# Kernel optimization log

Hardware: AMD Instinct MI355X
Metric: run time of the kernel (lower is better)

## Reference

```python
import jax, jax.numpy as jnp
import numpy as np

B, C_FEAT, H_F, W_F = 16, 256, 80, 80
C_ILL, K, H_Z, W_Z = 64, 3, 40, 40


def setup_inputs() -> dict:
    key = jax.random.key(0)
    k1, k2, k3, k4, k5, k6, k7 = jax.random.split(key, 7)
    feat = jax.random.normal(k1, (B, C_FEAT, H_F, W_F), dtype=jnp.float32)
    Z = jax.random.normal(k2, (B, C_ILL, H_Z, W_Z), dtype=jnp.float32)
    P = jax.random.uniform(k3, (B, K, H_Z, W_Z), dtype=jnp.float32)
    # Expert 1x1-conv params (original zero-inits; use small random for nontrivial math)
    Wg = jax.random.normal(k4, (K, C_FEAT, C_ILL), dtype=jnp.float32) * 0.02
    bg = jax.random.normal(k5, (K, C_FEAT), dtype=jnp.float32) * 0.02
    Wb = jax.random.normal(k6, (K, C_FEAT, C_ILL), dtype=jnp.float32) * 0.02
    bb = jax.random.normal(k7, (K, C_FEAT), dtype=jnp.float32) * 0.02
    return {"feat": feat, "Z": Z, "P": P, "Wg": Wg, "bg": bg, "Wb": Wb, "bb": bb}


def reference(feat, Z, P, Wg, bg, Wb, bb):
    Bb, C, H, W = feat.shape
    # bilinear upsample, half-pixel centers (== torch align_corners=False)
    Z_up = jax.image.resize(Z, (Z.shape[0], Z.shape[1], H, W), method='bilinear')
    P_up = jax.image.resize(P, (P.shape[0], P.shape[1], H, W), method='bilinear')
    # router-weighted illumination features: [B,K,D,H,W]
    ZP = jnp.einsum('bkhw,bdhw->bkdhw', P_up, Z_up)
    # soft-routed 1x1-conv experts, fused across K (weights + router-weighted biases)
    delta_gamma = jnp.einsum('bkdhw,kcd->bchw', ZP, Wg) + jnp.einsum('bkhw,kc->bchw', P_up, bg)
    delta_beta = jnp.einsum('bkdhw,kcd->bchw', ZP, Wb) + jnp.einsum('bkhw,kc->bchw', P_up, bb)
    # FiLM residual modulation
    return feat * (1.0 + delta_gamma) + delta_beta
```

## Files before the change

### kernel.cpp

```cpp
#include <hip/hip_runtime.h>
#include <hip/hip_bf16.h>

#define NB   16
#define NC   256
#define HF   80
#define WF   80
#define NPIX 6400
#define ND   64
#define NK   3
#define HZ   40
#define WZ   40
#define KD   224
#define NKC  7
#define NPB  400
#define ZP_B_STRIDE ((size_t)NPB * NKC * 512)
#define PB_STRIDE   (NKC * 512)
#define A_G_STRIDE  (NKC * 4 * 512)

typedef __bf16 bf16;
typedef __bf16 bf16x8 __attribute__((ext_vector_type(8)));
typedef float  floatx4 __attribute__((ext_vector_type(4)));

__global__ __launch_bounds__(256) void pack_A_kernel(
    const float* __restrict__ Wg, const float* __restrict__ bg,
    const float* __restrict__ Wb, const float* __restrict__ bb,
    bf16* __restrict__ A2)
{
    int i = blockIdx.x * 256 + threadIdx.x;
    int lane = i & 63;
    int j2 = i >> 6;
    int mt = j2 & 3;
    int j3 = j2 >> 2;
    int kc = j3 % 7;
    int g  = j3 / 7;
    int l15 = lane & 15, q = lane >> 4;
    int cbase = (g >> 1) * 64 + (g & 1) * 32;
    int c = cbase + (mt & 1) * 16 + l15;
    const float* W    = (mt >= 2) ? Wb : Wg;
    const float* bias = (mt >= 2) ? bb : bg;
    int kd0 = kc * 32 + q * 8;

    bf16x8 v;
    if (kd0 < NK * ND) {
        int k = kd0 >> 6, d = kd0 & 63;
        const float* src = W + ((size_t)k * NC + c) * ND + d;
        #pragma unroll
        for (int j = 0; j < 8; ++j) v[j] = (bf16)src[j];
    } else if (kd0 == NK * ND) {
        #pragma unroll
        for (int j = 0; j < 8; ++j) v[j] = (bf16)0.0f;
        v[0] = (bf16)bias[0 * NC + c];
        v[1] = (bf16)bias[1 * NC + c];
        v[2] = (bf16)bias[2 * NC + c];
    } else {
        #pragma unroll
        for (int j = 0; j < 8; ++j) v[j] = (bf16)0.0f;
    }
    *reinterpret_cast<bf16x8*>(A2 + (size_t)i * 8) = v;
}

__global__ __launch_bounds__(256) void build_zp_kernel(
    const float* __restrict__ Z, const float* __restrict__ P,
    bf16* __restrict__ ZP2)
{
    __shared__ float z_up[WF][ND + 1];
    __shared__ float p_up[WF][NK];

    const int bid = blockIdx.x;
    const int b   = bid / HF;
    const int h   = bid - b * HF;
    const int t   = threadIdx.x;

    float srch = 0.5f * (float)h - 0.25f;
    float flh  = floorf(srch);
    float fh   = srch - flh;
    int h0 = (int)flh, h1 = h0 + 1;
    h0 = max(h0, 0); h1 = min(h1, HZ - 1);

    #pragma unroll 4
    for (int i = 0; i < 20; ++i) {
        int e = t + 256 * i;
        int d = e / WF;
        int w = e - d * WF;
        float srcw = 0.5f * (float)w - 0.25f;
        float flw  = floorf(srcw);
        float fw   = srcw - flw;
        int w0 = (int)flw, w1 = w0 + 1;
        w0 = max(w0, 0); w1 = min(w1, WZ - 1);
        const float* Zr = Z + (size_t)(b * ND + d) * (HZ * WZ);
        float z00 = Zr[h0 * WZ + w0], z01 = Zr[h0 * WZ + w1];
        float z10 = Zr[h1 * WZ + w0], z11 = Zr[h1 * WZ + w1];
        float zi0 = z00 + fw * (z01 - z00);
        float zi1 = z10 + fw * (z11 - z10);
        z_up[w][d] = zi0 + fh * (zi1 - zi0);
    }
    if (t < WF * NK) {
        int w = t / NK;
        int k = t - w * NK;
        float srcw = 0.5f * (float)w - 0.25f;
        float flw  = floorf(srcw);
        float fw   = srcw - flw;
        int w0 = (int)flw, w1 = w0 + 1;
        w0 = max(w0, 0); w1 = min(w1, WZ - 1);
        const float* Pr = P + (size_t)(b * NK + k) * (HZ * WZ);
        float p00 = Pr[h0 * WZ + w0], p01 = Pr[h0 * WZ + w1];
        float p10 = Pr[h1 * WZ + w0], p11 = Pr[h1 * WZ + w1];
        float pi0 = p00 + fw * (p01 - p00);
        float pi1 = p10 + fw * (p11 - p10);
        p_up[w][k] = pi0 + fh * (pi1 - pi0);
    }
    __syncthreads();

    const size_t rowbase = (size_t)(b * (NPB * NKC) + h * 5 * NKC) * 512;
    for (int i = t; i < 5 * NKC * 64; i += 256) {
        int lane = i & 63;
        int j2   = i >> 6;
        int kc   = j2 % NKC;
        int pb_l = j2 / NKC;
        int l15 = lane & 15, q = lane >> 4;
        int w   = pb_l * 16 + l15;
        int kd0 = kc * 32 + q * 8;
        bf16x8 v;
        if (kd0 < NK * ND) {
            int k  = kd0 >> 6;
            int d0 = kd0 & 63;
            float p = p_up[w][k];
            #pragma unroll
            for (int j = 0; j < 8; ++j)
                v[j] = (bf16)(p * z_up[w][d0 + j]);
        } else if (kd0 == NK * ND) {
            #pragma unroll
            for (int j = 0; j < 8; ++j) v[j] = (bf16)0.0f;
            v[0] = (bf16)p_up[w][0];
            v[1] = (bf16)p_up[w][1];
            v[2] = (bf16)p_up[w][2];
        } else {
            #pragma unroll
            for (int j = 0; j < 8; ++j) v[j] = (bf16)0.0f;
        }
        *reinterpret_cast<bf16x8*>(ZP2 + rowbase + ((size_t)(pb_l * NKC + kc) * 64 + lane) * 8) = v;
    }
}

__global__ __launch_bounds__(256) void gemm_film_kernel(
    const bf16* __restrict__ A2, const bf16* __restrict__ ZP2,
    const float* __restrict__ feat, float* __restrict__ out)
{
    const int ntb = blockIdx.x;
    const int ct  = blockIdx.y;
    const int b   = blockIdx.z;
    const int tid  = threadIdx.x;
    const int lane = tid & 63;
    const int wv   = tid >> 6;
    const int mq   = wv & 1;
    const int nh   = wv >> 1;
    const int l15  = lane & 15;
    const int q    = lane >> 4;

    const int g     = ct * 2 + mq;
    const int cbase = ct * 64 + mq * 32;
    const int pb0   = ntb * 8 + nh * 4;
    const int pix0  = pb0 * 16;

    const bf16* aptr = A2 + (size_t)g * A_G_STRIDE + (size_t)lane * 8;
    const bf16* bptr = ZP2 + (size_t)b * ZP_B_STRIDE + (size_t)pb0 * PB_STRIDE
                       + (size_t)lane * 8;

    floatx4 acc[4][4] = {};

    for (int kc = 0; kc < NKC; ++kc) {
        bf16x8 af[4], bfr[4];
        #pragma unroll
        for (int mt = 0; mt < 4; ++mt)
            af[mt] = *reinterpret_cast<const bf16x8*>(aptr + mt * 512);
        #pragma unroll
        for (int nt = 0; nt < 4; ++nt)
            bfr[nt] = *reinterpret_cast<const bf16x8*>(bptr + nt * PB_STRIDE);
        aptr += 4 * 512;
        bptr += 512;
        #pragma unroll
        for (int mt = 0; mt < 4; ++mt)
            #pragma unroll
            for (int nt = 0; nt < 4; ++nt)
                acc[mt][nt] = __builtin_amdgcn_mfma_f32_16x16x32_bf16(
                    af[mt], bfr[nt], acc[mt][nt], 0, 0, 0);
    }

    const float* featb = feat + (size_t)b * NC * NPIX;
    float* outb = out + (size_t)b * NC * NPIX;
    #pragma unroll
    for (int mt = 0; mt < 2; ++mt) {
        #pragma unroll
        for (int r = 0; r < 4; ++r) {
            int c = cbase + mt * 16 + q * 4 + r;
            const float* frow = featb + (size_t)c * NPIX;
            float* orow = outb + (size_t)c * NPIX;
            #pragma unroll
            for (int nt = 0; nt < 4; ++nt) {
                int pix = pix0 + nt * 16 + l15;
                float gaccum = acc[mt][nt][r];
                float be     = acc[mt + 2][nt][r];
                float f      = frow[pix];
                orow[pix] = f * (1.0f + gaccum) + be;
            }
        }
    }
}

extern "C" void kernel_launch(void* const* d_in, const int* in_sizes, int n_in,
                              void* d_out, int out_size, void* d_ws, size_t ws_size,
                              hipStream_t stream)
{
    (void)in_sizes; (void)n_in; (void)out_size; (void)ws_size;
    const float* feat = (const float*)d_in[0];
    const float* Z    = (const float*)d_in[1];
    const float* P    = (const float*)d_in[2];
    const float* Wg   = (const float*)d_in[3];
    const float* bg   = (const float*)d_in[4];
    const float* Wb   = (const float*)d_in[5];
    const float* bb   = (const float*)d_in[6];

    bf16* ZPw = (bf16*)d_ws;
    bf16* Apk = ZPw + (size_t)NB * ZP_B_STRIDE;
    float* out = (float*)d_out;

    pack_A_kernel<<<56, 256, 0, stream>>>(Wg, bg, Wb, bb, Apk);
    build_zp_kernel<<<NB * HF, 256, 0, stream>>>(Z, P, ZPw);

    dim3 grid(NPIX / 128, NC / 64, NB);
    gemm_film_kernel<<<grid, 256, 0, stream>>>(Apk, ZPw, feat, out);
}
```

Before: 283.4 us.

## Fuse bilinear ZP construction into GEMM-FiLM kernel via shared memory

Drops the separate build_zp kernel and its global bf16 ZP workspace. Each block now upsamples Z and P for one image row into shared memory and runs the MFMA GEMM straight from LDS, with each wave covering 32 channels and 80 pixels. This removes the global write and re-read of the intermediate and one launch. The cost is that each row's upsampling is recomputed by two blocks (one per channel half), and LDS reads use a padded 232-element row stride.

```diff
diff --git a/kernel.cpp b/kernel.cpp
--- a/kernel.cpp
+++ b/kernel.cpp
@@ -10,11 +10,8 @@
 #define NK   3
 #define HZ   40
 #define WZ   40
-#define KD   224
 #define NKC  7
-#define NPB  400
-#define ZP_B_STRIDE ((size_t)NPB * NKC * 512)
-#define PB_STRIDE   (NKC * 512)
+#define ZROW 232
 #define A_G_STRIDE  (NKC * 4 * 512)
 
 typedef __bf16 bf16;
@@ -34,8 +31,7 @@
     int kc = j3 % 7;
     int g  = j3 / 7;
     int l15 = lane & 15, q = lane >> 4;
-    int cbase = (g >> 1) * 64 + (g & 1) * 32;
-    int c = cbase + (mt & 1) * 16 + l15;
+    int c = g * 32 + (mt & 1) * 16 + l15;
     const float* W    = (mt >= 2) ? Wb : Wg;
     const float* bias = (mt >= 2) ? bb : bg;
     int kd0 = kc * 32 + q * 8;
@@ -59,40 +55,36 @@
     *reinterpret_cast<bf16x8*>(A2 + (size_t)i * 8) = v;
 }
 
-__global__ __launch_bounds__(256) void build_zp_kernel(
-    const float* __restrict__ Z, const float* __restrict__ P,
-    bf16* __restrict__ ZP2)
+__global__ __launch_bounds__(256) void gemm_film_fused(
+    const bf16* __restrict__ A2, const float* __restrict__ Z,
+    const float* __restrict__ P, const float* __restrict__ feat,
+    float* __restrict__ out)
 {
-    __shared__ float z_up[WF][ND + 1];
+    __shared__ bf16  zp[WF * ZROW];
     __shared__ float p_up[WF][NK];
 
-    const int bid = blockIdx.x;
-    const int b   = bid / HF;
-    const int h   = bid - b * HF;
-    const int t   = threadIdx.x;
+    const int ct = blockIdx.x;
+    const int h  = blockIdx.y;
+    const int b  = blockIdx.z;
+    const int t    = threadIdx.x;
+    const int lane = t & 63;
+    const int wv   = t >> 6;
+    const int l15  = lane & 15;
+    const int q    = lane >> 4;
 
     float srch = 0.5f * (float)h - 0.25f;
     float flh  = floorf(srch);
     float fh   = srch - flh;
-    int h0 = (int)flh, h1 = h0 + 1;
-    h0 = max(h0, 0); h1 = min(h1, HZ - 1);
+    int h0 = max((int)flh, 0);
+    int h1 = min((int)flh + 1, HZ - 1);
 
-    #pragma unroll 4
-    for (int i = 0; i < 20; ++i) {
-        int e = t + 256 * i;
-        int d = e / WF;
-        int w = e - d * WF;
-        float srcw = 0.5f * (float)w - 0.25f;
-        float flw  = floorf(srcw);
-        float fw   = srcw - flw;
-        int w0 = (int)flw, w1 = w0 + 1;
-        w0 = max(w0, 0); w1 = min(w1, WZ - 1);
-        const float* Zr = Z + (size_t)(b * ND + d) * (HZ * WZ);
-        float z00 = Zr[h0 * WZ + w0], z01 = Zr[h0 * WZ + w1];
-        float z10 = Zr[h1 * WZ + w0], z11 = Zr[h1 * WZ + w1];
-        float zi0 = z00 + fw * (z01 - z00);
-        float zi1 = z10 + fw * (z11 - z10);
-        z_up[w][d] = zi0 + fh * (zi1 - zi0);
+    {
+        unsigned* zpu = (unsigned*)zp;
+        #pragma unroll
+        for (int i = t; i < WF * 16; i += 256) {
+            int w = i >> 4, j = i & 15;
+            zpu[w * 116 + 96 + j] = 0u;
+        }
     }
     if (t < WF * NK) {
         int w = t / NK;
@@ -100,8 +92,8 @@
         float srcw = 0.5f * (float)w - 0.25f;
         float flw  = floorf(srcw);
         float fw   = srcw - flw;
-        int w0 = (int)flw, w1 = w0 + 1;
-        w0 = max(w0, 0); w1 = min(w1, WZ - 1);
+        int w0 = max((int)flw, 0);
+        int w1 = min((int)flw + 1, WZ - 1);
         const float* Pr = P + (size_t)(b * NK + k) * (HZ * WZ);
         float p00 = Pr[h0 * WZ + w0], p01 = Pr[h0 * WZ + w1];
         float p10 = Pr[h1 * WZ + w0], p11 = Pr[h1 * WZ + w1];
@@ -111,97 +103,73 @@
     }
     __syncthreads();
 
-    const size_t rowbase = (size_t)(b * (NPB * NKC) + h * 5 * NKC) * 512;
-    for (int i = t; i < 5 * NKC * 64; i += 256) {
-        int lane = i & 63;
-        int j2   = i >> 6;
-        int kc   = j2 % NKC;
-        int pb_l = j2 / NKC;
-        int l15 = lane & 15, q = lane >> 4;
-        int w   = pb_l * 16 + l15;
-        int kd0 = kc * 32 + q * 8;
-        bf16x8 v;
-        if (kd0 < NK * ND) {
-            int k  = kd0 >> 6;
-            int d0 = kd0 & 63;
-            float p = p_up[w][k];
-            #pragma unroll
-            for (int j = 0; j < 8; ++j)
-                v[j] = (bf16)(p * z_up[w][d0 + j]);
-        } else if (kd0 == NK * ND) {
-            #pragma unroll
-            for (int j = 0; j < 8; ++j) v[j] = (bf16)0.0f;
-            v[0] = (bf16)p_up[w][0];
-            v[1] = (bf16)p_up[w][1];
-            v[2] = (bf16)p_up[w][2];
-        } else {
-            #pragma unroll
-            for (int j = 0; j < 8; ++j) v[j] = (bf16)0.0f;
-        }
-        *reinterpret_cast<bf16x8*>(ZP2 + rowbase + ((size_t)(pb_l * NKC + kc) * 64 + lane) * 8) = v;
+    if (t < WF * NK) {
+        int w = t / NK;
+        int k = t - w * NK;
+        zp[w * ZROW + NK * ND + k] = (bf16)p_up[w][k];
     }
-}
+    #pragma unroll 4
+    for (int i = 0; i < 20; ++i) {
+        int e = t + 256 * i;
+        int d = e / WF;
+        int w = e - d * WF;
+        float srcw = 0.5f * (float)w - 0.25f;
+        float flw  = floorf(srcw);
+        float fw   = srcw - flw;
+        int w0 = max((int)flw, 0);
+        int w1 = min((int)flw + 1, WZ - 1);
+        const float* Zr = Z + (size_t)(b * ND + d) * (HZ * WZ);
+        float z00 = Zr[h0 * WZ + w0], z01 = Zr[h0 * WZ + w1];
+        float z10 = Zr[h1 * WZ + w0], z11 = Zr[h1 * WZ + w1];
+        float zi0 = z00 + fw * (z01 - z00);
+        float zi1 = z10 + fw * (z11 - z10);
+        float zv  = zi0 + fh * (zi1 - zi0);
+        bf16* row = zp + w * ZROW;
+        row[d]            = (bf16)(p_up[w][0] * zv);
+        row[ND + d]       = (bf16)(p_up[w][1] * zv);
+        row[2 * ND + d]   = (bf16)(p_up[w][2] * zv);
+    }
+    __syncthreads();
 
-__global__ __launch_bounds__(256) void gemm_film_kernel(
-    const bf16* __restrict__ A2, const bf16* __restrict__ ZP2,
-    const float* __restrict__ feat, float* __restrict__ out)
-{
-    const int ntb = blockIdx.x;
-    const int ct  = blockIdx.y;
-    const int b   = blockIdx.z;
-    const int tid  = threadIdx.x;
-    const int lane = tid & 63;
-    const int wv   = tid >> 6;
-    const int mq   = wv & 1;
-    const int nh   = wv >> 1;
-    const int l15  = lane & 15;
-    const int q    = lane >> 4;
+    const int g = ct * 4 + wv;
+    const bf16* aptr = A2 + (size_t)g * A_G_STRIDE + (size_t)lane * 8;
 
-    const int g     = ct * 2 + mq;
-    const int cbase = ct * 64 + mq * 32;
-    const int pb0   = ntb * 8 + nh * 4;
-    const int pix0  = pb0 * 16;
-
-    const bf16* aptr = A2 + (size_t)g * A_G_STRIDE + (size_t)lane * 8;
-    const bf16* bptr = ZP2 + (size_t)b * ZP_B_STRIDE + (size_t)pb0 * PB_STRIDE
-                       + (size_t)lane * 8;
-
-    floatx4 acc[4][4] = {};
+    floatx4 acc[4][5] = {};
 
     for (int kc = 0; kc < NKC; ++kc) {
-        bf16x8 af[4], bfr[4];
+        bf16x8 af[4];
         #pragma unroll
         for (int mt = 0; mt < 4; ++mt)
             af[mt] = *reinterpret_cast<const bf16x8*>(aptr + mt * 512);
+        aptr += 4 * 512;
+        const int kd0 = kc * 32 + q * 8;
         #pragma unroll
-        for (int nt = 0; nt < 4; ++nt)
-            bfr[nt] = *reinterpret_cast<const bf16x8*>(bptr + nt * PB_STRIDE);
-        aptr += 4 * 512;
-        bptr += 512;
-        #pragma unroll
-        for (int mt = 0; mt < 4; ++mt)
+        for (int nt = 0; nt < 5; ++nt) {
+            bf16x8 bfr = *reinterpret_cast<const bf16x8*>(
+                zp + (nt * 16 + l15) * ZROW + kd0);
             #pragma unroll
-            for (int nt = 0; nt < 4; ++nt)
+            for (int mt = 0; mt < 4; ++mt)
                 acc[mt][nt] = __builtin_amdgcn_mfma_f32_16x16x32_bf16(
-                    af[mt], bfr[nt], acc[mt][nt], 0, 0, 0);
+                    af[mt], bfr, acc[mt][nt], 0, 0, 0);
+        }
     }
 
-    const float* featb = feat + (size_t)b * NC * NPIX;
-    float* outb = out + (size_t)b * NC * NPIX;
+    const int cbase = g * 32;
+    const size_t imgbase = (size_t)b * NC * NPIX + (size_t)h * WF;
     #pragma unroll
     for (int mt = 0; mt < 2; ++mt) {
         #pragma unroll
         for (int r = 0; r < 4; ++r) {
             int c = cbase + mt * 16 + q * 4 + r;
-            const float* frow = featb + (size_t)c * NPIX;
-            float* orow = outb + (size_t)c * NPIX;
+            const float* frow = feat + imgbase + (size_t)c * NPIX;
+            float*       orow = out  + imgbase + (size_t)c * NPIX;
             #pragma unroll
-            for (int nt = 0; nt < 4; ++nt) {
-                int pix = pix0 + nt * 16 + l15;
-                float gaccum = acc[mt][nt][r];
-                float be     = acc[mt + 2][nt][r];
-                float f      = frow[pix];
-                orow[pix] = f * (1.0f + gaccum) + be;
+            for (int nt = 0; nt < 5; ++nt) {
+                int pix = nt * 16 + l15;
+                float ga = acc[mt][nt][r];
+                float be = acc[mt + 2][nt][r];
+                float f  = frow[pix];
+                orow[pix] = f * (1.0f + ga) + be;
             }
         }
     }
@@ -220,13 +188,11 @@
     const float* Wb   = (const float*)d_in[5];
     const float* bb   = (const float*)d_in[6];
 
-    bf16* ZPw = (bf16*)d_ws;
-    bf16* Apk = ZPw + (size_t)NB * ZP_B_STRIDE;
+    bf16* Apk = (bf16*)d_ws;
     float* out = (float*)d_out;
 
     pack_A_kernel<<<56, 256, 0, stream>>>(Wg, bg, Wb, bb, Apk);
-    build_zp_kernel<<<NB * HF, 256, 0, stream>>>(Z, P, ZPw);
 
-    dim3 grid(NPIX / 128, NC / 64, NB);
-    gemm_film_kernel<<<grid, 256, 0, stream>>>(Apk, ZPw, feat, out);
+    dim3 grid(2, HF, NB);
+    gemm_film_fused<<<grid, 256, 0, stream>>>(Apk, Z, P, feat, out);
 }
```

Measured after the change: 300.8 us. 6.1% more time.
